# Optimization experiments

Hardware: AMD Instinct MI355X
Metric: run time of the kernel (lower is better)

The kernel has to match this reference:

```python
import jax, jax.numpy as jnp
from jax import lax
import numpy as np

N, C, H, W = 8, 128, 96, 96
G, K = 8, 3                      # groups, kernel_size
GC = C // G                      # group channels = 16
STRIDE, PAD, DIL = 1, 1, 1
OFFSET_SCALE = 1.0
OM_DIM = int(np.ceil(G * K * K * 3 / 8) * 8)   # 216 (== G*K*K*3, no padding)
GN_EPS = 1e-5


def setup_inputs() -> dict:
    key = jax.random.key(0)
    ks = jax.random.split(key, 7)
    inp = {
        "input": jax.random.normal(ks[0], (N, C, H, W), dtype=jnp.float32),
        # depthwise conv (Conv2d groups=C): OIHW with I=1
        "dw_w": jax.random.normal(ks[1], (C, 1, K, K), dtype=jnp.float32) * 0.1,
        "dw_b": jax.random.normal(ks[2], (C,), dtype=jnp.float32) * 0.05,
        # GroupNorm(num_groups=1) affine params
        "gn_w": jnp.ones((C,), dtype=jnp.float32),
        "gn_b": jnp.zeros((C,), dtype=jnp.float32),
        # offset_mask Linear (module zero-inits; use small random for a meaningful test)
        "om_w": jax.random.normal(ks[3], (OM_DIM, C), dtype=jnp.float32) * 0.02,
        "om_b": jax.random.normal(ks[4], (OM_DIM,), dtype=jnp.float32) * 0.02,
    }
    return inp


def _dcnv4_forward(x, dw_w, dw_b, gn_w, gn_b, om_w, om_b):
    # x: (N, C, H, W)
    # ---- offset/mask branch: depthwise conv -> GroupNorm(1) -> GELU -> Linear
    x1 = lax.conv_general_dilated(
        x, dw_w, window_strides=(1, 1), padding=[(1, 1), (1, 1)],
        feature_group_count=C, dimension_numbers=("NCHW", "OIHW", "NCHW"))
    x1 = x1 + dw_b[None, :, None, None]
    mu = jnp.mean(x1, axis=(1, 2, 3), keepdims=True)
    var = jnp.var(x1, axis=(1, 2, 3), keepdims=True)
    x1 = (x1 - mu) * lax.rsqrt(var + GN_EPS)
    x1 = x1 * gn_w[None, :, None, None] + gn_b[None, :, None, None]
    x1 = jax.nn.gelu(x1, approximate=False)
    x1 = jnp.transpose(x1, (0, 2, 3, 1))                     # (N,H,W,C)
    om = jnp.einsum("nhwc,oc->nhwo", x1, om_w) + om_b        # (N,H,W,216)

    K2 = K * K
    om = om[..., : G * K2 * 3].reshape(N, H, W, G, K2 * 3)
    offs = om[..., : 2 * K2].reshape(N, H, W, G, K2, 2)      # (dx, dy) per point
    mask = om[..., 2 * K2:]                                  # (N,H,W,G,K2), no softmax in DCNv4

    # ---- sampling locations (pixel coords in the unpadded input, zeros outside)
    ky, kx = jnp.meshgrid(jnp.arange(K), jnp.arange(K), indexing="ij")
    base_y = ((ky - (K - 1) / 2.0) * DIL).reshape(-1).astype(jnp.float32)  # (K2,)
    base_x = ((kx - (K - 1) / 2.0) * DIL).reshape(-1).astype(jnp.float32)
    ctr_y = jnp.arange(H, dtype=jnp.float32) * STRIDE - PAD + DIL * (K - 1) / 2.0
    ctr_x = jnp.arange(W, dtype=jnp.float32) * STRIDE - PAD + DIL * (K - 1) / 2.0
    loc_y = ctr_y[None, :, None, None, None] + (base_y + offs[..., 1]) * OFFSET_SCALE
    loc_x = ctr_x[None, None, :, None, None] + (base_x + offs[..., 0]) * OFFSET_SCALE

    # ---- grouped bilinear gather
    xv = jnp.transpose(x, (0, 2, 3, 1)).reshape(N, H, W, G, GC)   # values, channels-last
    y0 = jnp.floor(loc_y)
    x0 = jnp.floor(loc_x)
    ly = loc_y - y0
    lx = loc_x - x0
    y0i = y0.astype(jnp.int32)
    x0i = x0.astype(jnp.int32)
    n_idx = jnp.arange(N)[:, None, None, None, None]
    g_idx = jnp.arange(G)[None, None, None, :, None]

    def gather(yi, xi):
        valid = (yi >= 0) & (yi < H) & (xi >= 0) & (xi < W)
        yc = jnp.clip(yi, 0, H - 1)
        xc = jnp.clip(xi, 0, W - 1)
        v = xv[n_idx, yc, xc, g_idx]                 # (N,H,W,G,K2,GC)
        return v * valid[..., None].astype(xv.dtype)

    samp = (gather(y0i,     x0i)     * ((1 - ly) * (1 - lx))[..., None]
          + gather(y0i,     x0i + 1) * ((1 - ly) * lx)[..., None]
          + gather(y0i + 1, x0i)     * (ly * (1 - lx))[..., None]
          + gather(y0i + 1, x0i + 1) * (ly * lx)[..., None])

    out = jnp.sum(samp * mask[..., None], axis=4)    # (N,H,W,G,GC)
    out = out.reshape(N, H, W, C)
    return jnp.transpose(out, (0, 3, 1, 2))          # (N,C,H,W)


def reference(input, dw_w, dw_b, gn_w, gn_b, om_w, om_b):
    return _dcnv4_forward(input, dw_w, dw_b, gn_w, gn_b, om_w, om_b)
```

## Files before the change

### kernel.cpp

```cpp
#include <hip/hip_runtime.h>

#define N_   8
#define C_   128
#define H_   96
#define W_   96
#define G_   8
#define GC_  16
#define HW_  (H_ * W_)
#define CHW_ (C_ * HW_)
#define OM_  216
#define OMP_ 224
#define OMROWS2_ 112
#define EPS_ 1e-5f
#define BLKS_PER_N_ 192

typedef short bf16x8 __attribute__((ext_vector_type(8)));
typedef float f32x4 __attribute__((ext_vector_type(4)));

#if __has_builtin(__builtin_amdgcn_fdot2_f32_bf16)
#define HAVE_DOT2_ 1
typedef __bf16 bf16x2 __attribute__((ext_vector_type(2)));
static __device__ __forceinline__ bf16x2 u2bf2(unsigned int u) {
  union { unsigned int i; bf16x2 v; } c;
  c.i = u;
  return c.v;
}
#else
#define HAVE_DOT2_ 0
#endif

static __device__ __forceinline__ unsigned short f2bf(float f) {
  unsigned int u = __float_as_uint(f);
  unsigned int r = (u + 0x7fffu + ((u >> 16) & 1u)) >> 16;
  return (unsigned short)r;
}
static __device__ __forceinline__ float lo_bf(unsigned int u) {
  return __uint_as_float(u << 16);
}
static __device__ __forceinline__ float hi_bf(unsigned int u) {
  return __uint_as_float(u & 0xffff0000u);
}

static __device__ __forceinline__ float fast_gelu(float z) {
  float s = z * 0.70710678118654752f;
  float as = fabsf(s);
  float t = __builtin_amdgcn_rcpf(fmaf(0.3275911f, as, 1.0f));
  float e = __expf(-as * as);
  float inner = fmaf(fmaf(fmaf(fmaf(1.061405429f, t, -1.453152027f), t,
                               1.421413741f), t, -0.284496736f), t, 0.254829592f);
  float y = fmaf(-inner * t, e, 1.0f);
  float erf_s = copysignf(y, s);
  float hz = 0.5f * z;
  return fmaf(hz, erf_s, hz);
}

static __device__ __forceinline__ void loadrow5(float dst[2][5],
                                                const float* __restrict__ xp0,
                                                const float* __restrict__ xp1,
                                                int hh, int w0) {
  bool vy = (hh >= 0) & (hh < H_);
#pragma unroll
  for (int j = 0; j < 5; ++j) {
    int ww = w0 - 1 + j;
    bool v = vy & (ww >= 0) & (ww < W_);
    dst[0][j] = v ? xp0[hh * W_ + ww] : 0.0f;
    dst[1][j] = v ? xp1[hh * W_ + ww] : 0.0f;
  }
}

__global__ __launch_bounds__(256) void k_front(const float* __restrict__ x,
                                               const float* __restrict__ dw_w,
                                               const float* __restrict__ dw_b,
                                               unsigned short* __restrict__ xgb,
                                               unsigned short* __restrict__ x1b,
                                               float2* __restrict__ partials) {
  __shared__ unsigned int lds_c[384 * 9];
  __shared__ unsigned int lds_a[384 * 9];
  __shared__ float ls[4], lq[4];

  int tx = threadIdx.x;
  int ty = threadIdx.y;
  int tid = ty * 32 + tx;
  int hb = blockIdx.x;
  int g  = blockIdx.y;
  int n  = blockIdx.z;
  int h0 = hb * 4;
  int w0 = tx * 3;

  const int c0 = g * 16 + 2 * ty;
  float wk[2][9];
  const float* wp = dw_w + c0 * 9;
#pragma unroll
  for (int j = 0; j < 9; ++j) {
    wk[0][j] = wp[j];
    wk[1][j] = wp[9 + j];
  }
  float bias[2] = {dw_b[c0], dw_b[c0 + 1]};

  const float* xp0 = x + ((size_t)(n * C_ + c0)) * HW_;
  const float* xp1 = xp0 + HW_;

  float s = 0.0f, q = 0.0f;

  float rr[3][2][5];
  loadrow5(rr[0], xp0, xp1, h0 - 1, w0);
  loadrow5(rr[1], xp0, xp1, h0,     w0);

#pragma unroll
  for (int r = 0; r < 4; ++r) {
    const int sA = r % 3;
    const int sB = (r + 1) % 3;
    const int sC = (r + 2) % 3;
    loadrow5(rr[sC], xp0, xp1, h0 + r + 1, w0);

#pragma unroll
    for (int j = 0; j < 3; ++j) {
      float acc0 = bias[0], acc1 = bias[1];
#pragma unroll
      for (int dx = 0; dx < 3; ++dx) {
        acc0 = fmaf(rr[sA][0][j + dx], wk[0][0 + dx], acc0);
        acc1 = fmaf(rr[sA][1][j + dx], wk[1][0 + dx], acc1);
        acc0 = fmaf(rr[sB][0][j + dx], wk[0][3 + dx], acc0);
        acc1 = fmaf(rr[sB][1][j + dx], wk[1][3 + dx], acc1);
        acc0 = fmaf(rr[sC][0][j + dx], wk[0][6 + dx], acc0);
        acc1 = fmaf(rr[sC][1][j + dx], wk[1][6 + dx], acc1);
      }
      float cen0 = rr[sB][0][j + 1];
      float cen1 = rr[sB][1][j + 1];
      s += acc0 + acc1;
      q = fmaf(acc0, acc0, q);
      q = fmaf(acc1, acc1, q);
      int pxl = r * 96 + w0 + j;
      lds_a[pxl * 9 + ty] = (unsigned int)f2bf(acc0) |
                            ((unsigned int)f2bf(acc1) << 16);
      lds_c[pxl * 9 + ty] = (unsigned int)f2bf(cen0) |
                            ((unsigned int)f2bf(cen1) << 16);
    }
  }
  __syncthreads();

  for (int i = tid; i < 384; i += 256) {
    int p = h0 * W_ + i;
    unsigned int wc[8], wa[8];
#pragma unroll
    for (int k = 0; k < 8; ++k) {
      wc[k] = lds_c[i * 9 + k];
      wa[k] = lds_a[i * 9 + k];
    }
    unsigned int* xg = (unsigned int*)xgb + ((size_t)(n * G_ + g) * HW_ + p) * 8;
    uint4 c01 = {wc[0], wc[1], wc[2], wc[3]};
    uint4 c23 = {wc[4], wc[5], wc[6], wc[7]};
    *(uint4*)xg = c01;
    *(uint4*)(xg + 4) = c23;
    unsigned int* xb = (unsigned int*)x1b + ((size_t)n * HW_ + p) * 64 + g * 8;
    uint4 a01 = {wa[0], wa[1], wa[2], wa[3]};
    uint4 a23 = {wa[4], wa[5], wa[6], wa[7]};
    *(uint4*)xb = a01;
    *(uint4*)(xb + 4) = a23;
  }

#pragma unroll
  for (int o = 32; o > 0; o >>= 1) {
    s += __shfl_down(s, o);
    q += __shfl_down(q, o);
  }
  int lane = tid & 63;
  int wv = tid >> 6;
  if (lane == 0) { ls[wv] = s; lq[wv] = q; }
  __syncthreads();
  if (tid == 0) {
    int bid = hb + 24 * g + BLKS_PER_N_ * n;
    partials[bid] = make_float2(ls[0] + ls[1] + ls[2] + ls[3],
                                lq[0] + lq[1] + lq[2] + lq[3]);
  }
}

__global__ __launch_bounds__(256) void k_prep(const float* __restrict__ om_w,
                                              const float* __restrict__ om_b,
                                              unsigned short* __restrict__ A,
                                              float* __restrict__ biasp) {
  int idx = blockIdx.x * 256 + threadIdx.x;
  int o = idx >> 7;
  int cix = idx & 127;
  int g = o / 28;
  int k = o - g * 28;
  float v = (k < 27) ? om_w[(g * 27 + k) * C_ + cix] : 0.0f;
  A[idx] = f2bf(v);
  if (cix == 0) biasp[o] = (k < 27) ? om_b[g * 27 + k] : 0.0f;
}

__global__ __launch_bounds__(256) void k_gemm_mfma(const unsigned short* __restrict__ Bt,
                                                   const unsigned short* __restrict__ A,
                                                   const float* __restrict__ biasp,
                                                   const float2* __restrict__ partials,
                                                   const float* __restrict__ gn_w,
                                                   const float* __restrict__ gn_b,
                                                   unsigned int* __restrict__ om2) {
  __shared__ unsigned short Bl[32 * 136];
  __shared__ alignas(16) float s_bias[OMP_];
  __shared__ float ls[4], lq[4];
  int tid = threadIdx.x;
  int pb = blockIdx.x;
  int n = blockIdx.y;
  int p0 = pb * 32;

  {
    float s = 0.0f, q = 0.0f;
    if (tid < BLKS_PER_N_) {
      float2 v = partials[n * BLKS_PER_N_ + tid];
      s = v.x;
      q = v.y;
    }
#pragma unroll
    for (int o = 32; o > 0; o >>= 1) {
      s += __shfl_down(s, o);
      q += __shfl_down(q, o);
    }
    int lane = tid & 63;
    int wv = tid >> 6;
    if (lane == 0) { ls[wv] = s; lq[wv] = q; }
  }
  if (tid < OMP_ / 4) {
    ((float4*)s_bias)[tid] = ((const float4*)biasp)[tid];
  }
  __syncthreads();

  float sum = ls[0] + ls[1] + ls[2] + ls[3];
  float ssq = lq[0] + lq[1] + lq[2] + lq[3];
  const float inv = 1.0f / (float)CHW_;
  float mean = sum * inv;
  float var = ssq * inv - mean * mean;
  float rstd = rsqrtf(var + EPS_);
  int cbase = (tid & 15) * 8;
  float a8[8], b8[8];
#pragma unroll
  for (int j = 0; j < 8; ++j) {
    float gw = gn_w[cbase + j];
    float gb = gn_b[cbase + j];
    a8[j] = rstd * gw;
    b8[j] = gb - mean * rstd * gw;
  }

  const unsigned short* src = Bt + ((size_t)n * HW_ + p0) * C_;
#pragma unroll
  for (int i = 0; i < 2; ++i) {
    int idx = i * 256 + tid;
    int row = idx >> 4;
    int col = idx & 15;
    uint4 raw = *(const uint4*)(src + row * C_ + col * 8);
    unsigned int d[4] = {raw.x, raw.y, raw.z, raw.w};
    unsigned int od[4];
#pragma unroll
    for (int t = 0; t < 4; ++t) {
      float v0 = lo_bf(d[t]);
      float v1 = hi_bf(d[t]);
      float z0 = fmaf(v0, a8[2 * t], b8[2 * t]);
      float z1 = fmaf(v1, a8[2 * t + 1], b8[2 * t + 1]);
      float g0 = fast_gelu(z0);
      float g1 = fast_gelu(z1);
      od[t] = (unsigned int)f2bf(g0) | ((unsigned int)f2bf(g1) << 16);
    }
    uint4 packed = {od[0], od[1], od[2], od[3]};
    *(uint4*)(&Bl[row * 136 + col * 8]) = packed;
  }
  __syncthreads();

  int wave = tid >> 6;
  int lane = tid & 63;
  int quad = lane >> 4;
  int l16 = lane & 15;
  int pixhalf = wave & 1;
  int othalf = wave >> 1;
  int prow = pixhalf * 16 + l16;

  bf16x8 bfrag[4];
#pragma unroll
  for (int kk = 0; kk < 4; ++kk)
    bfrag[kk] = *(const bf16x8*)(&Bl[prow * 136 + kk * 32 + quad * 8]);

  int p = p0 + prow;
  for (int oi = 0; oi < 7; ++oi) {
    int ot = othalf * 7 + oi;
    const unsigned short* Ap = A + (ot * 16 + l16) * C_ + quad * 8;
    bf16x8 afrag[4];
#pragma unroll
    for (int kk = 0; kk < 4; ++kk)
      afrag[kk] = *(const bf16x8*)(Ap + kk * 32);

    f32x4 acc = {0.f, 0.f, 0.f, 0.f};
#pragma unroll
    for (int kk = 0; kk < 4; ++kk)
      acc = __builtin_amdgcn_mfma_f32_16x16x32_bf16(afrag[kk], bfrag[kk], acc, 0, 0, 0);

    int o0 = ot * 16 + quad * 4;
    float4 bv = *(const float4*)(&s_bias[o0]);
    unsigned int pk0 = (unsigned int)f2bf(acc[0] + bv.x) |
                       ((unsigned int)f2bf(acc[1] + bv.y) << 16);
    unsigned int pk1 = (unsigned int)f2bf(acc[2] + bv.z) |
                       ((unsigned int)f2bf(acc[3] + bv.w) << 16);
    unsigned int* Cp = om2 + ((size_t)n * OMROWS2_ + (o0 >> 1)) * HW_ + p;
    Cp[0] = pk0;
    Cp[HW_] = pk1;
  }
}

__global__ __launch_bounds__(256) void k_sample(const unsigned short* __restrict__ xgb,
                                                const unsigned int* __restrict__ om2,
                                                float* __restrict__ out) {
  __shared__ int4 s_wa[9 * 64];

  int tid = threadIdx.x;
  int ord = blockIdx.x;
  int n = ord & 7;
  int t2 = ord >> 3;
  int g = t2 & 7;
  int pb = t2 >> 3;
  int p0 = pb * 64;

  const unsigned int* omb = om2 + ((size_t)n * OMROWS2_ + g * 14) * HW_ + p0;
  for (int j = tid; j < 576; j += 256) {
    int pt = j >> 6;
    int px = j & 63;
    int p = p0 + px;
    int h = p / W_;
    int w = p - h * W_;
    unsigned int od = omb[pt * HW_ + px];
    float offx = lo_bf(od);
    float offy = hi_bf(od);
    unsigned int md = omb[(9 + (pt >> 1)) * HW_ + px];
    float m = (pt & 1) ? hi_bf(md) : lo_bf(md);
    float locy = (float)(h + pt / 3 - 1) + offy;
    float locx = (float)(w + pt % 3 - 1) + offx;
    float y0f = floorf(locy);
    float x0f = floorf(locx);
    float ly = locy - y0f;
    float lx = locx - x0f;
    int y0 = (int)y0f;
    int x0 = (int)x0f;
    int y1 = y0 + 1;
    int x1 = x0 + 1;
    bool vy0 = (y0 >= 0) & (y0 < H_);
    bool vy1 = (y1 >= 0) & (y1 < H_);
    bool vx0 = (x0 >= 0) & (x0 < W_);
    bool vx1 = (x1 >= 0) & (x1 < W_);
    float t0 = (1.0f - ly) * m;
    float t1 = ly * m;
    float u0 = 1.0f - lx;
    float w00 = (vy0 & vx0) ? t0 * u0 : 0.0f;
    float w01 = (vy0 & vx1) ? t0 * lx : 0.0f;
    float w10 = (vy1 & vx0) ? t1 * u0 : 0.0f;
    float w11 = (vy1 & vx1) ? t1 * lx : 0.0f;
    int yc0 = min(max(y0, 0), H_ - 1);
    int yc1 = min(max(y1, 0), H_ - 1);
    int xs  = min(max(x0, 0), W_ - 2);
    int idx0 = min(max(x0, 0), W_ - 1) - xs;
    int idx1 = min(max(x1, 0), W_ - 1) - xs;
    float wr0y0 = (idx0 == 0 ? w00 : 0.0f) + (idx1 == 0 ? w01 : 0.0f);
    float wr1y0 = (idx0 == 1 ? w00 : 0.0f) + (idx1 == 1 ? w01 : 0.0f);
    float wr0y1 = (idx0 == 0 ? w10 : 0.0f) + (idx1 == 0 ? w11 : 0.0f);
    float wr1y1 = (idx0 == 1 ? w10 : 0.0f) + (idx1 == 1 ? w11 : 0.0f);
    int4 wa;
    wa.x = (int)((unsigned int)f2bf(wr0y0) | ((unsigned int)f2bf(wr0y1) << 16));
    wa.y = (int)((unsigned int)f2bf(wr1y0) | ((unsigned int)f2bf(wr1y1) << 16));
    wa.z = (yc0 * W_ + xs) * GC_;
    wa.w = (yc1 * W_ + xs) * GC_;
    s_wa[j] = wa;
  }
  __syncthreads();

  int px_l = tid >> 2;
  int sub = tid & 3;
  int rowhalf = sub >> 1;
  int chunk = sub & 1;
  int p = p0 + px_l;
  const unsigned short* xbb = xgb + ((size_t)(n * G_ + g) * HW_) * GC_;

  float acc[8] = {0, 0, 0, 0, 0, 0, 0, 0};
#pragma unroll
  for (int pt = 0; pt < 9; ++pt) {
    int4 wa = s_wa[pt * 64 + px_l];
    unsigned int aw = (unsigned int)(rowhalf ? wa.y : wa.x);
    uint4 r0 = *(const uint4*)(xbb + wa.z + sub * 8);
    uint4 r1 = *(const uint4*)(xbb + wa.w + sub * 8);
    unsigned int d0[4] = {r0.x, r0.y, r0.z, r0.w};
    unsigned int d1[4] = {r1.x, r1.y, r1.z, r1.w};
#if HAVE_DOT2_
    bf16x2 a2 = u2bf2(aw);
#pragma unroll
    for (int t = 0; t < 4; ++t) {
      unsigned int blo = __builtin_amdgcn_perm(d1[t], d0[t], 0x05040100u);
      unsigned int bhi = __builtin_amdgcn_perm(d1[t], d0[t], 0x07060302u);
      acc[2 * t]     = __builtin_amdgcn_fdot2_f32_bf16(a2, u2bf2(blo), acc[2 * t], false);
      acc[2 * t + 1] = __builtin_amdgcn_fdot2_f32_bf16(a2, u2bf2(bhi), acc[2 * t + 1], false);
    }
#else
    float w0 = lo_bf(aw);
    float w1 = hi_bf(aw);
#pragma unroll
    for (int t = 0; t < 4; ++t) {
      acc[2 * t]     = fmaf(w0, lo_bf(d0[t]), acc[2 * t]);
      acc[2 * t + 1] = fmaf(w0, hi_bf(d0[t]), acc[2 * t + 1]);
      acc[2 * t]     = fmaf(w1, lo_bf(d1[t]), acc[2 * t]);
      acc[2 * t + 1] = fmaf(w1, hi_bf(d1[t]), acc[2 * t + 1]);
    }
#endif
  }

#pragma unroll
  for (int i = 0; i < 8; ++i) acc[i] += __shfl_xor(acc[i], 2);

  int ch = chunk * 8 + rowhalf * 4;
  float* op = out + ((size_t)(n * C_ + g * GC_ + ch)) * HW_ + p;
#pragma unroll
  for (int r = 0; r < 4; ++r) op[r * HW_] = acc[rowhalf * 4 + r];
}

extern "C" void kernel_launch(void* const* d_in, const int* in_sizes, int n_in,
                              void* d_out, int out_size, void* d_ws, size_t ws_size,
                              hipStream_t stream) {
  const float* x    = (const float*)d_in[0];
  const float* dw_w = (const float*)d_in[1];
  const float* dw_b = (const float*)d_in[2];
  const float* gn_w = (const float*)d_in[3];
  const float* gn_b = (const float*)d_in[4];
  const float* om_w = (const float*)d_in[5];
  const float* om_b = (const float*)d_in[6];
  float* out = (float*)d_out;

  unsigned short* xgb = (unsigned short*)d_ws;
  unsigned short* x1b = xgb + (size_t)N_ * CHW_;
  unsigned int* om2 = (unsigned int*)(x1b + (size_t)N_ * CHW_);
  float* stats = (float*)(om2 + (size_t)N_ * OMROWS2_ * HW_);
  float2* partials = (float2*)(stats + 16);
  unsigned short* Abf = (unsigned short*)(partials + N_ * BLKS_PER_N_);
  float* biasp = (float*)(Abf + OMP_ * C_);

  k_prep<<<(OMP_ * C_) / 256, 256, 0, stream>>>(om_w, om_b, Abf, biasp);
  k_front<<<dim3(24, G_, N_), dim3(32, 8), 0, stream>>>(
      x, dw_w, dw_b, xgb, x1b, partials);
  k_gemm_mfma<<<dim3(HW_ / 32, N_), 256, 0, stream>>>(
      x1b, Abf, biasp, partials, gn_w, gn_b, om2);
  k_sample<<<9216, 256, 0, stream>>>(xgb, om2, out);
}
```

Baseline: 184.2 us.

## Store sampled values in zero-padded planes to drop bounds checks in sampler

```diff
diff --git a/kernel.cpp b/kernel.cpp
--- a/kernel.cpp
+++ b/kernel.cpp
@@ -1,4 +1,5 @@
 #include <hip/hip_runtime.h>
+#include <hip/hip_bf16.h>
 
 #define N_   8
 #define C_   128
@@ -13,6 +14,8 @@
 #define OMROWS2_ 112
 #define EPS_ 1e-5f
 #define BLKS_PER_N_ 192
+#define PW_  100
+#define PPLANE_ (PW_ * PW_ * GC_)
 
 typedef short bf16x8 __attribute__((ext_vector_type(8)));
 typedef float f32x4 __attribute__((ext_vector_type(4)));
@@ -33,6 +36,12 @@
   unsigned int u = __float_as_uint(f);
   unsigned int r = (u + 0x7fffu + ((u >> 16) & 1u)) >> 16;
   return (unsigned short)r;
+}
+static __device__ __forceinline__ unsigned int pk_bf2(float lo, float hi) {
+  __hip_bfloat162 h = __float22bfloat162_rn(make_float2(lo, hi));
+  union { __hip_bfloat162 h; unsigned int u; } c;
+  c.h = h;
+  return c.u;
 }
 static __device__ __forceinline__ float lo_bf(unsigned int u) {
   return __uint_as_float(u << 16);
@@ -131,27 +140,28 @@
       q = fmaf(acc0, acc0, q);
       q = fmaf(acc1, acc1, q);
       int pxl = r * 96 + w0 + j;
-      lds_a[pxl * 9 + ty] = (unsigned int)f2bf(acc0) |
-                            ((unsigned int)f2bf(acc1) << 16);
-      lds_c[pxl * 9 + ty] = (unsigned int)f2bf(cen0) |
-                            ((unsigned int)f2bf(cen1) << 16);
+      lds_a[pxl * 9 + ty] = pk_bf2(acc0, acc1);
+      lds_c[pxl * 9 + ty] = pk_bf2(cen0, cen1);
     }
   }
   __syncthreads();
 
   for (int i = tid; i < 384; i += 256) {
-    int p = h0 * W_ + i;
+    int row = i / 96;
+    int col = i - row * 96;
     unsigned int wc[8], wa[8];
 #pragma unroll
     for (int k = 0; k < 8; ++k) {
       wc[k] = lds_c[i * 9 + k];
       wa[k] = lds_a[i * 9 + k];
     }
-    unsigned int* xg = (unsigned int*)xgb + ((size_t)(n * G_ + g) * HW_ + p) * 8;
+    unsigned int* xg = (unsigned int*)xgb + (size_t)(n * G_ + g) * (PPLANE_ / 2)
+                       + ((h0 + row + 2) * PW_ + (col + 2)) * 8;
     uint4 c01 = {wc[0], wc[1], wc[2], wc[3]};
     uint4 c23 = {wc[4], wc[5], wc[6], wc[7]};
     *(uint4*)xg = c01;
     *(uint4*)(xg + 4) = c23;
+    int p = (h0 + row) * W_ + col;
     unsigned int* xb = (unsigned int*)x1b + ((size_t)n * HW_ + p) * 64 + g * 8;
     uint4 a01 = {wa[0], wa[1], wa[2], wa[3]};
     uint4 a23 = {wa[4], wa[5], wa[6], wa[7]};
@@ -178,15 +188,43 @@
 __global__ __launch_bounds__(256) void k_prep(const float* __restrict__ om_w,
                                               const float* __restrict__ om_b,
                                               unsigned short* __restrict__ A,
-                                              float* __restrict__ biasp) {
-  int idx = blockIdx.x * 256 + threadIdx.x;
-  int o = idx >> 7;
-  int cix = idx & 127;
-  int g = o / 28;
-  int k = o - g * 28;
-  float v = (k < 27) ? om_w[(g * 27 + k) * C_ + cix] : 0.0f;
-  A[idx] = f2bf(v);
-  if (cix == 0) biasp[o] = (k < 27) ? om_b[g * 27 + k] : 0.0f;
+                                              float* __restrict__ biasp,
+                                              unsigned short* __restrict__ xgb) {
+  int b = blockIdx.x;
+  int tid = threadIdx.x;
+  if (b < 112) {
+    int idx = b * 256 + tid;
+    int o = idx >> 7;
+    int cix = idx & 127;
+    int g = o / 28;
+    int k = o - g * 28;
+    float v = (k < 27) ? om_w[(g * 27 + k) * C_ + cix] : 0.0f;
+    A[idx] = f2bf(v);
+    if (cix == 0) biasp[o] = (k < 27) ? om_b[g * 27 + k] : 0.0f;
+  } else {
+    int gid = (b - 112) * 256 + tid;
+    const int NBORD = 64 * 784;
+    for (int id = gid; id < NBORD; id += 80 * 256) {
+      int plane = id / 784;
+      int r = id - plane * 784;
+      int row, col;
+      if (r < 400) {
+        int qq = r / 100;
+        row = (qq < 2) ? qq : qq + 96;
+        col = r - qq * 100;
+      } else {
+        int r2 = r - 400;
+        int qq = r2 >> 2;
+        int c4 = r2 & 3;
+        row = 2 + qq;
+        col = (c4 < 2) ? c4 : c4 + 96;
+      }
+      uint4* dst = (uint4*)(xgb + (size_t)plane * PPLANE_ + (row * PW_ + col) * GC_);
+      uint4 z = {0, 0, 0, 0};
+      dst[0] = z;
+      dst[1] = z;
+    }
+  }
 }
 
 __global__ __launch_bounds__(256) void k_gemm_mfma(const unsigned short* __restrict__ Bt,
@@ -256,9 +294,7 @@
       float v1 = hi_bf(d[t]);
       float z0 = fmaf(v0, a8[2 * t], b8[2 * t]);
       float z1 = fmaf(v1, a8[2 * t + 1], b8[2 * t + 1]);
-      float g0 = fast_gelu(z0);
-      float g1 = fast_gelu(z1);
-      od[t] = (unsigned int)f2bf(g0) | ((unsigned int)f2bf(g1) << 16);
+      od[t] = pk_bf2(fast_gelu(z0), fast_gelu(z1));
     }
     uint4 packed = {od[0], od[1], od[2], od[3]};
     *(uint4*)(&Bl[row * 136 + col * 8]) = packed;
@@ -294,10 +330,8 @@
 
     int o0 = ot * 16 + quad * 4;
     float4 bv = *(const float4*)(&s_bias[o0]);
-    unsigned int pk0 = (unsigned int)f2bf(acc[0] + bv.x) |
-                       ((unsigned int)f2bf(acc[1] + bv.y) << 16);
-    unsigned int pk1 = (unsigned int)f2bf(acc[2] + bv.z) |
-                       ((unsigned int)f2bf(acc[3] + bv.w) << 16);
+    unsigned int pk0 = pk_bf2(acc[0] + bv.x, acc[1] + bv.y);
+    unsigned int pk1 = pk_bf2(acc[2] + bv.z, acc[3] + bv.w);
     unsigned int* Cp = om2 + ((size_t)n * OMROWS2_ + (o0 >> 1)) * HW_ + p;
     Cp[0] = pk0;
     Cp[HW_] = pk1;
@@ -337,33 +371,16 @@
     float lx = locx - x0f;
     int y0 = (int)y0f;
     int x0 = (int)x0f;
-    int y1 = y0 + 1;
-    int x1 = x0 + 1;
-    bool vy0 = (y0 >= 0) & (y0 < H_);
-    bool vy1 = (y1 >= 0) & (y1 < H_);
-    bool vx0 = (x0 >= 0) & (x0 < W_);
-    bool vx1 = (x1 >= 0) & (x1 < W_);
+    y0 = min(max(y0, -2), 96);
+    x0 = min(max(x0, -2), 96);
     float t0 = (1.0f - ly) * m;
     float t1 = ly * m;
     float u0 = 1.0f - lx;
-    float w00 = (vy0 & vx0) ? t0 * u0 : 0.0f;
-    float w01 = (vy0 & vx1) ? t0 * lx : 0.0f;
-    float w10 = (vy1 & vx0) ? t1 * u0 : 0.0f;
-    float w11 = (vy1 & vx1) ? t1 * lx : 0.0f;
-    int yc0 = min(max(y0, 0), H_ - 1);
-    int yc1 = min(max(y1, 0), H_ - 1);
-    int xs  = min(max(x0, 0), W_ - 2);
-    int idx0 = min(max(x0, 0), W_ - 1) - xs;
-    int idx1 = min(max(x1, 0), W_ - 1) - xs;
-    float wr0y0 = (idx0 == 0 ? w00 : 0.0f) + (idx1 == 0 ? w01 : 0.0f);
-    float wr1y0 = (idx0 == 1 ? w00 : 0.0f) + (idx1 == 1 ? w01 : 0.0f);
-    float wr0y1 = (idx0 == 0 ? w10 : 0.0f) + (idx1 == 0 ? w11 : 0.0f);
-    float wr1y1 = (idx0 == 1 ? w10 : 0.0f) + (idx1 == 1 ? w11 : 0.0f);
     int4 wa;
-    wa.x = (int)((unsigned int)f2bf(wr0y0) | ((unsigned int)f2bf(wr0y1) << 16));
-    wa.y = (int)((unsigned int)f2bf(wr1y0) | ((unsigned int)f2bf(wr1y1) << 16));
-    wa.z = (yc0 * W_ + xs) * GC_;
-    wa.w = (yc1 * W_ + xs) * GC_;
+    wa.x = (int)pk_bf2(t0 * u0, t1 * u0);
+    wa.y = (int)pk_bf2(t0 * lx, t1 * lx);
+    wa.z = ((y0 + 2) * PW_ + (x0 + 2)) * GC_;
+    wa.w = wa.z + PW_ * GC_;
     s_wa[j] = wa;
   }
   __syncthreads();
@@ -373,7 +390,7 @@
   int rowhalf = sub >> 1;
   int chunk = sub & 1;
   int p = p0 + px_l;
-  const unsigned short* xbb = xgb + ((size_t)(n * G_ + g) * HW_) * GC_;
+  const unsigned short* xbb = xgb + (size_t)(n * G_ + g) * PPLANE_;
 
   float acc[8] = {0, 0, 0, 0, 0, 0, 0, 0};
 #pragma unroll
@@ -428,14 +445,14 @@
   float* out = (float*)d_out;
 
   unsigned short* xgb = (unsigned short*)d_ws;
-  unsigned short* x1b = xgb + (size_t)N_ * CHW_;
+  unsigned short* x1b = xgb + (size_t)64 * PPLANE_;
   unsigned int* om2 = (unsigned int*)(x1b + (size_t)N_ * CHW_);
   float* stats = (float*)(om2 + (size_t)N_ * OMROWS2_ * HW_);
   float2* partials = (float2*)(stats + 16);
   unsigned short* Abf = (unsigned short*)(partials + N_ * BLKS_PER_N_);
   float* biasp = (float*)(Abf + OMP_ * C_);
 
-  k_prep<<<(OMP_ * C_) / 256, 256, 0, stream>>>(om_w, om_b, Abf, biasp);
+  k_prep<<<192, 256, 0, stream>>>(om_w, om_b, Abf, biasp, xgb);
   k_front<<<dim3(24, G_, N_), dim3(32, 8), 0, stream>>>(
       x, dw_w, dw_b, xgb, x1b, partials);
   k_gemm_mfma<<<dim3(HW_ / 32, N_), 256, 0, stream>>>(
```

After: 181.7 us. About the same (-1.4%).
